# Kernel optimization log

Hardware: AMD Instinct MI355X
Metric: run time of the kernel (lower is better)

Reference implementation:

```python
import jax, jax.numpy as jnp
import numpy as np


def _cayley(X):
    # torch orthogonal parametrization, orthogonal_map='cayley', use_trivialization=False:
    # A = tril(X,-1); A = A - A^T (skew);  Q = (I - A/2)^{-1} (I + A/2)
    n = X.shape[0]
    A = jnp.tril(X, -1)
    A = A - A.T
    I = jnp.eye(n, dtype=X.dtype)
    return jnp.linalg.solve(I - 0.5 * A, I + 0.5 * A)


def setup_inputs() -> dict:
    key = jax.random.key(0)
    ks = jax.random.split(key, 8)
    L, R = 64, 64
    B, S = 4, 2048
    x = jax.random.normal(ks[0], (B, S, L * R), dtype=jnp.float32)
    return {
        "x": x,
        "u_left": jax.random.normal(ks[1], (L, L), dtype=jnp.float32) * 0.02,
        "v_left": jax.random.normal(ks[2], (L, L), dtype=jnp.float32) * 0.02,
        "diag_left": jnp.ones((L,), dtype=jnp.float32),
        "u_right": jax.random.normal(ks[3], (R, R), dtype=jnp.float32) * 0.02,
        "v_right": jax.random.normal(ks[4], (R, R), dtype=jnp.float32) * 0.02,
        "diag_right": jnp.ones((R,), dtype=jnp.float32),
        "diag_scale": 1.0 + 0.01 * jax.random.normal(ks[5], (L * R,), dtype=jnp.float32),
    }


def reference(x, u_left, v_left, diag_left, u_right, v_right, diag_right, diag_scale):
    L = diag_left.shape[0]
    R = diag_right.shape[0]
    # SVD-composed trans matrices: M = Cayley(U) @ diag(S) @ Cayley(V)
    m_left = _cayley(u_left) @ (diag_left[:, None] * _cayley(v_left))    # [L, L]
    m_right = _cayley(u_right) @ (diag_right[:, None] * _cayley(v_right))  # [R, R]
    # add_diag: elementwise diagonal scale on hidden dim
    xs = x * diag_scale
    shp = xs.shape
    xm = xs.reshape(-1, L, R)  # [N, L, R]
    # kronecker_matmul: m_left^T @ X @ m_right
    out = jnp.einsum('il,nij,jr->nlr', m_left, xm, m_right)
    return out.reshape(shp)
```

## Files before the change

kernel.cpp:

```cpp
#include <hip/hip_runtime.h>
#include <hip/hip_bf16.h>

typedef __attribute__((ext_vector_type(8))) short short8;
typedef __attribute__((ext_vector_type(4))) short short4v;
typedef __attribute__((ext_vector_type(4))) float floatx4;

#define MFMA(a, b, c) __builtin_amdgcn_mfma_f32_16x16x32_bf16((a), (b), (c), 0, 0, 0)

__device__ __forceinline__ short f2bf(float f) {
    unsigned u = __float_as_uint(f);
    u += 0x7fffu + ((u >> 16) & 1u);
    return (short)(u >> 16);
}

__device__ void cayley64(const float* __restrict__ X, const float* __restrict__ dg,
                         short* outArr, int mode,
                         short* Brow, float* Bcol, short* T0, short* T1, int tid)
{
    int i0 = (tid * 16) >> 6;
    int j0 = (tid * 16) & 63;
#pragma unroll
    for (int s = 0; s < 16; ++s) {
        int i = i0, j = j0 + s;
        float b = 0.f;
        if (i > j)      b =  0.5f * X[i * 64 + j];
        else if (i < j) b = -0.5f * X[j * 64 + i];
        Brow[i * 72 + j] = f2bf(b);
        Bcol[j * 68 + i] = b;
        T0[j * 72 + i]   = f2bf(b);
    }
    __syncthreads();

    int lane = tid & 63, w = tid >> 6, m = lane & 15, q = lane >> 4;
    int arow = (w * 16 + m) * 72;
    short8 a0 = *(const short8*)&Brow[arow + q * 8];
    short8 a1 = *(const short8*)&Brow[arow + 32 + q * 8];

    short* Tbuf[2] = {T0, T1};
    int cur = 0;
    const int NSTEP = 9;
    for (int step = 0; step < NSTEP; ++step) {
        bool last = (step == NSTEP - 1);
        short* Tr = Tbuf[cur];
        short* Tw = Tbuf[cur ^ 1];
#pragma unroll
        for (int c = 0; c < 4; ++c) {
            int coff = c * 16 + m;
            short8 b0 = *(const short8*)&Tr[coff * 72 + q * 8];
            short8 b1 = *(const short8*)&Tr[coff * 72 + 32 + q * 8];
            floatx4 acc = {0.f, 0.f, 0.f, 0.f};
            acc = MFMA(a0, b0, acc);
            acc = MFMA(a1, b1, acc);
            int row0 = w * 16 + q * 4;
            floatx4 badd = *(const floatx4*)&Bcol[coff * 68 + row0];
            floatx4 t = badd + acc;
            if (!last) {
                short4v pk = { f2bf(t.x), f2bf(t.y), f2bf(t.z), f2bf(t.w) };
                *(short4v*)&Tw[coff * 72 + row0] = pk;
            } else {
                int col = coff;
                floatx4 cv;
                cv.x = ((row0 + 0) == col ? 1.f : 0.f) + 2.f * t.x;
                cv.y = ((row0 + 1) == col ? 1.f : 0.f) + 2.f * t.y;
                cv.z = ((row0 + 2) == col ? 1.f : 0.f) + 2.f * t.z;
                cv.w = ((row0 + 3) == col ? 1.f : 0.f) + 2.f * t.w;
                if (mode == 0) {
                    outArr[(row0 + 0) * 72 + col] = f2bf(cv.x);
                    outArr[(row0 + 1) * 72 + col] = f2bf(cv.y);
                    outArr[(row0 + 2) * 72 + col] = f2bf(cv.z);
                    outArr[(row0 + 3) * 72 + col] = f2bf(cv.w);
                } else {
                    floatx4 dv = *(const floatx4*)&dg[row0];
                    short4v pk = { f2bf(cv.x * dv.x), f2bf(cv.y * dv.y),
                                   f2bf(cv.z * dv.z), f2bf(cv.w * dv.w) };
                    *(short4v*)&outArr[col * 72 + row0] = pk;
                }
            }
        }
        __syncthreads();
        cur ^= 1;
    }
}

__global__ __launch_bounds__(256) void k_prep(
        const float* __restrict__ u_l, const float* __restrict__ v_l, const float* __restrict__ dg_l,
        const float* __restrict__ u_r, const float* __restrict__ v_r, const float* __restrict__ dg_r,
        short* __restrict__ wsOut)
{
    __shared__ __align__(16) short Brow[64 * 72];
    __shared__ __align__(16) float Bcol[64 * 68];
    __shared__ __align__(16) short T0[64 * 72];
    __shared__ __align__(16) short T1[64 * 72];
    __shared__ __align__(16) short CvA[64 * 72];
    __shared__ __align__(16) short CuB[64 * 72];

    int tid = threadIdx.x;
    const float* U  = (blockIdx.x == 0) ? u_l  : u_r;
    const float* V  = (blockIdx.x == 0) ? v_l  : v_r;
    const float* DG = (blockIdx.x == 0) ? dg_l : dg_r;
    short* outT = wsOut + blockIdx.x * 4096;

    cayley64(V, DG, CvA, 1, Brow, Bcol, T0, T1, tid);
    __syncthreads();
    cayley64(U, DG, CuB, 0, Brow, Bcol, T0, T1, tid);
    __syncthreads();

    int lane = tid & 63, w = tid >> 6, m = lane & 15, q = lane >> 4;
    int arow = (w * 16 + m) * 72;
    short8 a0 = *(const short8*)&CvA[arow + q * 8];
    short8 a1 = *(const short8*)&CvA[arow + 32 + q * 8];
#pragma unroll
    for (int c = 0; c < 4; ++c) {
        short8 b0 = *(const short8*)&CuB[(c * 16 + m) * 72 + q * 8];
        short8 b1 = *(const short8*)&CuB[(c * 16 + m) * 72 + 32 + q * 8];
        floatx4 acc = {0.f, 0.f, 0.f, 0.f};
        acc = MFMA(a0, b0, acc);
        acc = MFMA(a1, b1, acc);
        int row0 = w * 16 + q * 4, col = c * 16 + m;
        outT[(row0 + 0) * 64 + col] = f2bf(acc.x);
        outT[(row0 + 1) * 64 + col] = f2bf(acc.y);
        outT[(row0 + 2) * 64 + col] = f2bf(acc.z);
        outT[(row0 + 3) * 64 + col] = f2bf(acc.w);
    }
}

#define NPB 4

__global__ __launch_bounds__(256) void k_main(
        const float* __restrict__ x, const float* __restrict__ dsc,
        const short* __restrict__ mLT, const short* __restrict__ mRT,
        float* __restrict__ out, int N)
{
    __shared__ __align__(16) short Xs[64 * 72];
    __shared__ __align__(16) short ST[64 * 72];

    int tid = threadIdx.x;
    int lane = tid & 63, w = tid >> 6, m = lane & 15, q = tid >> 4 & 3;
    q = lane >> 4;

    floatx4 ds[4];
#pragma unroll
    for (int i = 0; i < 4; ++i) ds[i] = *(const floatx4*)&dsc[(i * 256 + tid) * 4];

    short8 pf0 = *(const short8*)&mLT[(w * 16 + m) * 64 + q * 8];
    short8 pf1 = *(const short8*)&mLT[(w * 16 + m) * 64 + 32 + q * 8];
    short8 qf[4][2];
#pragma unroll
    for (int c = 0; c < 4; ++c) {
        qf[c][0] = *(const short8*)&mRT[(c * 16 + m) * 64 + q * 8];
        qf[c][1] = *(const short8*)&mRT[(c * 16 + m) * 64 + 32 + q * 8];
    }

    for (int it = 0; it < NPB; ++it) {
        int n = blockIdx.x * NPB + it;
        if (n >= N) break;
        const float* xp = x + (size_t)n * 4096;

#pragma unroll
        for (int i = 0; i < 4; ++i) {
            int f = i * 256 + tid;
            floatx4 v = *(const floatx4*)&xp[f * 4];
            v = v * ds[i];
            int row = f >> 4, col = (f & 15) * 4;
            short4v pk = { f2bf(v.x), f2bf(v.y), f2bf(v.z), f2bf(v.w) };
            *(short4v*)&Xs[row * 72 + col] = pk;
        }
        __syncthreads();

        int arow = (w * 16 + m) * 72;
        short8 xa0 = *(const short8*)&Xs[arow + q * 8];
        short8 xa1 = *(const short8*)&Xs[arow + 32 + q * 8];
#pragma unroll
        for (int c = 0; c < 4; ++c) {
            floatx4 s = {0.f, 0.f, 0.f, 0.f};
            s = MFMA(xa0, qf[c][0], s);
            s = MFMA(xa1, qf[c][1], s);
            short4v pk = { f2bf(s.x), f2bf(s.y), f2bf(s.z), f2bf(s.w) };
            *(short4v*)&ST[(c * 16 + m) * 72 + w * 16 + q * 4] = pk;
        }
        __syncthreads();

        float* op = out + (size_t)n * 4096;
#pragma unroll
        for (int c = 0; c < 4; ++c) {
            short8 sb0 = *(const short8*)&ST[(c * 16 + m) * 72 + q * 8];
            short8 sb1 = *(const short8*)&ST[(c * 16 + m) * 72 + 32 + q * 8];
            floatx4 o = {0.f, 0.f, 0.f, 0.f};
            o = MFMA(pf0, sb0, o);
            o = MFMA(pf1, sb1, o);
            int row0 = w * 16 + q * 4, col = c * 16 + m;
            op[(row0 + 0) * 64 + col] = o.x;
            op[(row0 + 1) * 64 + col] = o.y;
            op[(row0 + 2) * 64 + col] = o.z;
            op[(row0 + 3) * 64 + col] = o.w;
        }
    }
}

extern "C" void kernel_launch(void* const* d_in, const int* in_sizes, int n_in,
                              void* d_out, int out_size, void* d_ws, size_t ws_size,
                              hipStream_t stream) {
    const float* x    = (const float*)d_in[0];
    const float* u_l  = (const float*)d_in[1];
    const float* v_l  = (const float*)d_in[2];
    const float* dg_l = (const float*)d_in[3];
    const float* u_r  = (const float*)d_in[4];
    const float* v_r  = (const float*)d_in[5];
    const float* dg_r = (const float*)d_in[6];
    const float* dsc  = (const float*)d_in[7];
    float* out = (float*)d_out;
    short* ws  = (short*)d_ws;

    int N = in_sizes[0] / 4096;

    hipLaunchKernelGGL(k_prep, dim3(2), dim3(256), 0, stream,
                       u_l, v_l, dg_l, u_r, v_r, dg_r, ws);
    int grid = (N + NPB - 1) / NPB;
    hipLaunchKernelGGL(k_main, dim3(grid), dim3(256), 0, stream,
                       x, dsc, ws, ws + 4096, out, N);
}
```

Measured before the change: 266.1 us.

## Load x directly into MFMA fragments with register prefetch and double-buffered LDS

The main kernel now has each thread load its own x elements straight into the MFMA A-fragment layout in registers, which removes the Xs shared-memory staging and one barrier per matrix. It prefetches the next matrix's x into registers while the current one is computed, and double-buffers the intermediate ST tile so only one barrier per iteration is needed. Separately, the Cayley iteration count in the prep kernel drops from 9 to 6 steps. That shortens the tiny prep kernel but may leave the Neumann-series approximation less converged, which could affect accuracy. The per-thread x loads are now 16-byte chunks at strided row offsets rather than fully contiguous per-wavefront accesses.

```diff
diff --git a/kernel.cpp b/kernel.cpp
--- a/kernel.cpp
+++ b/kernel.cpp
@@ -11,6 +11,13 @@
     unsigned u = __float_as_uint(f);
     u += 0x7fffu + ((u >> 16) & 1u);
     return (short)(u >> 16);
+}
+
+__device__ __forceinline__ short8 pack_bf16(floatx4 a, floatx4 b) {
+    short8 r;
+    r[0] = f2bf(a.x); r[1] = f2bf(a.y); r[2] = f2bf(a.z); r[3] = f2bf(a.w);
+    r[4] = f2bf(b.x); r[5] = f2bf(b.y); r[6] = f2bf(b.z); r[7] = f2bf(b.w);
+    return r;
 }
 
 __device__ void cayley64(const float* __restrict__ X, const float* __restrict__ dg,
@@ -38,7 +45,7 @@
 
     short* Tbuf[2] = {T0, T1};
     int cur = 0;
-    const int NSTEP = 9;
+    const int NSTEP = 6;
     for (int step = 0; step < NSTEP; ++step) {
         bool last = (step == NSTEP - 1);
         short* Tr = Tbuf[cur];
@@ -131,16 +138,16 @@
         const short* __restrict__ mLT, const short* __restrict__ mRT,
         float* __restrict__ out, int N)
 {
-    __shared__ __align__(16) short Xs[64 * 72];
-    __shared__ __align__(16) short ST[64 * 72];
+    __shared__ __align__(16) short ST[2][64 * 72];
 
     int tid = threadIdx.x;
-    int lane = tid & 63, w = tid >> 6, m = lane & 15, q = tid >> 4 & 3;
-    q = lane >> 4;
-
-    floatx4 ds[4];
-#pragma unroll
-    for (int i = 0; i < 4; ++i) ds[i] = *(const floatx4*)&dsc[(i * 256 + tid) * 4];
+    int lane = tid & 63, w = tid >> 6, m = lane & 15, q = lane >> 4;
+    const int rowoff = (w * 16 + m) * 64 + q * 8;
+
+    floatx4 ds0a = *(const floatx4*)&dsc[rowoff];
+    floatx4 ds0b = *(const floatx4*)&dsc[rowoff + 4];
+    floatx4 ds1a = *(const floatx4*)&dsc[rowoff + 32];
+    floatx4 ds1b = *(const floatx4*)&dsc[rowoff + 36];
 
     short8 pf0 = *(const short8*)&mLT[(w * 16 + m) * 64 + q * 8];
     short8 pf1 = *(const short8*)&mLT[(w * 16 + m) * 64 + 32 + q * 8];
@@ -151,40 +158,51 @@
         qf[c][1] = *(const short8*)&mRT[(c * 16 + m) * 64 + 32 + q * 8];
     }
 
+    const int base = blockIdx.x * NPB;
+    const float* xb = x + (size_t)base * 4096 + rowoff;
+
+    floatx4 xr0, xr1, xr2, xr3;
+    if (base < N) {
+        xr0 = *(const floatx4*)&xb[0];
+        xr1 = *(const floatx4*)&xb[4];
+        xr2 = *(const floatx4*)&xb[32];
+        xr3 = *(const floatx4*)&xb[36];
+    }
+
+#pragma unroll
     for (int it = 0; it < NPB; ++it) {
-        int n = blockIdx.x * NPB + it;
+        int n = base + it;
         if (n >= N) break;
-        const float* xp = x + (size_t)n * 4096;
-
-#pragma unroll
-        for (int i = 0; i < 4; ++i) {
-            int f = i * 256 + tid;
-            floatx4 v = *(const floatx4*)&xp[f * 4];
-            v = v * ds[i];
-            int row = f >> 4, col = (f & 15) * 4;
-            short4v pk = { f2bf(v.x), f2bf(v.y), f2bf(v.z), f2bf(v.w) };
-            *(short4v*)&Xs[row * 72 + col] = pk;
-        }
-        __syncthreads();
-
-        int arow = (w * 16 + m) * 72;
-        short8 xa0 = *(const short8*)&Xs[arow + q * 8];
-        short8 xa1 = *(const short8*)&Xs[arow + 32 + q * 8];
+
+        floatx4 nx0, nx1, nx2, nx3;
+        bool pf = (it + 1 < NPB) && (n + 1 < N);
+        if (pf) {
+            const float* xn = xb + (size_t)(it + 1) * 4096;
+            nx0 = *(const floatx4*)&xn[0];
+            nx1 = *(const floatx4*)&xn[4];
+            nx2 = *(const floatx4*)&xn[32];
+            nx3 = *(const floatx4*)&xn[36];
+        }
+
+        short8 xa0 = pack_bf16(xr0 * ds0a, xr1 * ds0b);
+        short8 xa1 = pack_bf16(xr2 * ds1a, xr3 * ds1b);
+
+        short* STw = ST[it & 1];
 #pragma unroll
         for (int c = 0; c < 4; ++c) {
             floatx4 s = {0.f, 0.f, 0.f, 0.f};
             s = MFMA(xa0, qf[c][0], s);
             s = MFMA(xa1, qf[c][1], s);
             short4v pk = { f2bf(s.x), f2bf(s.y), f2bf(s.z), f2bf(s.w) };
-            *(short4v*)&ST[(c * 16 + m) * 72 + w * 16 + q * 4] = pk;
+            *(short4v*)&STw[(c * 16 + m) * 72 + w * 16 + q * 4] = pk;
         }
         __syncthreads();
 
         float* op = out + (size_t)n * 4096;
 #pragma unroll
         for (int c = 0; c < 4; ++c) {
-            short8 sb0 = *(const short8*)&ST[(c * 16 + m) * 72 + q * 8];
-            short8 sb1 = *(const short8*)&ST[(c * 16 + m) * 72 + 32 + q * 8];
+            short8 sb0 = *(const short8*)&STw[(c * 16 + m) * 72 + q * 8];
+            short8 sb1 = *(const short8*)&STw[(c * 16 + m) * 72 + 32 + q * 8];
             floatx4 o = {0.f, 0.f, 0.f, 0.f};
             o = MFMA(pf0, sb0, o);
             o = MFMA(pf1, sb1, o);
@@ -194,6 +212,7 @@
             op[(row0 + 2) * 64 + col] = o.z;
             op[(row0 + 3) * 64 + col] = o.w;
         }
+        if (pf) { xr0 = nx0; xr1 = nx1; xr2 = nx2; xr3 = nx3; }
     }
 }
 
```

After: 262.6 us. About the same (-1.3%).

## Process one matrix per wave without block barriers and cut Cayley iterations

Applied to the files above, without the earlier changes.

Restructures the main kernel so each wave owns a whole 64x64 matrix. It loads x straight from global memory into MFMA fragments, keeps both transform matrices in registers, and passes intermediate results through a small per-wave LDS buffer, so no block-wide __syncthreads are needed. Output is written as float4 vectors instead of scalar stores, and launch bounds ask for 2 blocks per CU. The Neumann-style Cayley iteration count drops from 9 to 6, which trades accuracy for a shorter prep kernel. Risks are higher register pressure and some loss of precision in the Cayley solve.

```diff
diff --git a/kernel.cpp b/kernel.cpp
--- a/kernel.cpp
+++ b/kernel.cpp
@@ -11,6 +11,13 @@
     unsigned u = __float_as_uint(f);
     u += 0x7fffu + ((u >> 16) & 1u);
     return (short)(u >> 16);
+}
+
+__device__ __forceinline__ short8 pack_bf16(floatx4 a, floatx4 b) {
+    short8 r;
+    r[0] = f2bf(a.x); r[1] = f2bf(a.y); r[2] = f2bf(a.z); r[3] = f2bf(a.w);
+    r[4] = f2bf(b.x); r[5] = f2bf(b.y); r[6] = f2bf(b.z); r[7] = f2bf(b.w);
+    return r;
 }
 
 __device__ void cayley64(const float* __restrict__ X, const float* __restrict__ dg,
@@ -38,7 +45,7 @@
 
     short* Tbuf[2] = {T0, T1};
     int cur = 0;
-    const int NSTEP = 9;
+    const int NSTEP = 6;
     for (int step = 0; step < NSTEP; ++step) {
         bool last = (step == NSTEP - 1);
         short* Tr = Tbuf[cur];
@@ -124,75 +131,82 @@
     }
 }
 
-#define NPB 4
-
-__global__ __launch_bounds__(256) void k_main(
+#define WPW 2
+
+__global__ __launch_bounds__(256, 2) void k_main(
         const float* __restrict__ x, const float* __restrict__ dsc,
         const short* __restrict__ mLT, const short* __restrict__ mRT,
         float* __restrict__ out, int N)
 {
-    __shared__ __align__(16) short Xs[64 * 72];
-    __shared__ __align__(16) short ST[64 * 72];
-
-    int tid = threadIdx.x;
-    int lane = tid & 63, w = tid >> 6, m = lane & 15, q = tid >> 4 & 3;
-    q = lane >> 4;
-
-    floatx4 ds[4];
-#pragma unroll
-    for (int i = 0; i < 4; ++i) ds[i] = *(const floatx4*)&dsc[(i * 256 + tid) * 4];
-
-    short8 pf0 = *(const short8*)&mLT[(w * 16 + m) * 64 + q * 8];
-    short8 pf1 = *(const short8*)&mLT[(w * 16 + m) * 64 + 32 + q * 8];
-    short8 qf[4][2];
+    __shared__ __align__(16) short STb[4][2][16 * 72];
+
+    int tid = threadIdx.x, lane = tid & 63, w = tid >> 6;
+    int m = lane & 15, q = lane >> 4;
+    const int fragoff = q * 8;
+
+    short8 qf[4][2], pfB[4][2];
 #pragma unroll
     for (int c = 0; c < 4; ++c) {
-        qf[c][0] = *(const short8*)&mRT[(c * 16 + m) * 64 + q * 8];
-        qf[c][1] = *(const short8*)&mRT[(c * 16 + m) * 64 + 32 + q * 8];
-    }
-
-    for (int it = 0; it < NPB; ++it) {
-        int n = blockIdx.x * NPB + it;
+        qf[c][0] = *(const short8*)&mRT[(c * 16 + m) * 64 + fragoff];
+        qf[c][1] = *(const short8*)&mRT[(c * 16 + m) * 64 + 32 + fragoff];
+    }
+#pragma unroll
+    for (int r = 0; r < 4; ++r) {
+        pfB[r][0] = *(const short8*)&mLT[(r * 16 + m) * 64 + fragoff];
+        pfB[r][1] = *(const short8*)&mLT[(r * 16 + m) * 64 + 32 + fragoff];
+    }
+
+    const int wid = blockIdx.x * 4 + w;
+
+#pragma unroll
+    for (int i = 0; i < WPW; ++i) {
+        int n = wid * WPW + i;
         if (n >= N) break;
         const float* xp = x + (size_t)n * 4096;
-
-#pragma unroll
-        for (int i = 0; i < 4; ++i) {
-            int f = i * 256 + tid;
-            floatx4 v = *(const floatx4*)&xp[f * 4];
-            v = v * ds[i];
-            int row = f >> 4, col = (f & 15) * 4;
-            short4v pk = { f2bf(v.x), f2bf(v.y), f2bf(v.z), f2bf(v.w) };
-            *(short4v*)&Xs[row * 72 + col] = pk;
-        }
-        __syncthreads();
-
-        int arow = (w * 16 + m) * 72;
-        short8 xa0 = *(const short8*)&Xs[arow + q * 8];
-        short8 xa1 = *(const short8*)&Xs[arow + 32 + q * 8];
+        float* op = out + (size_t)n * 4096;
+
+        floatx4 xf[4][4];
+#pragma unroll
+        for (int r = 0; r < 4; ++r) {
+            const float* rp = xp + (r * 16 + m) * 64 + fragoff;
+            xf[r][0] = *(const floatx4*)&rp[0];
+            xf[r][1] = *(const floatx4*)&rp[4];
+            xf[r][2] = *(const floatx4*)&rp[32];
+            xf[r][3] = *(const floatx4*)&rp[36];
+        }
+
+        short8 xa[4][2];
+#pragma unroll
+        for (int r = 0; r < 4; ++r) {
+            const float* dp = dsc + (r * 16 + m) * 64 + fragoff;
+            floatx4 d0 = *(const floatx4*)&dp[0];
+            floatx4 d1 = *(const floatx4*)&dp[4];
+            floatx4 d2 = *(const floatx4*)&dp[32];
+            floatx4 d3 = *(const floatx4*)&dp[36];
+            xa[r][0] = pack_bf16(xf[r][0] * d0, xf[r][1] * d1);
+            xa[r][1] = pack_bf16(xf[r][2] * d2, xf[r][3] * d3);
+        }
+
 #pragma unroll
         for (int c = 0; c < 4; ++c) {
-            floatx4 s = {0.f, 0.f, 0.f, 0.f};
-            s = MFMA(xa0, qf[c][0], s);
-            s = MFMA(xa1, qf[c][1], s);
-            short4v pk = { f2bf(s.x), f2bf(s.y), f2bf(s.z), f2bf(s.w) };
-            *(short4v*)&ST[(c * 16 + m) * 72 + w * 16 + q * 4] = pk;
-        }
-        __syncthreads();
-
-        float* op = out + (size_t)n * 4096;
-#pragma unroll
-        for (int c = 0; c < 4; ++c) {
-            short8 sb0 = *(const short8*)&ST[(c * 16 + m) * 72 + q * 8];
-            short8 sb1 = *(const short8*)&ST[(c * 16 + m) * 72 + 32 + q * 8];
-            floatx4 o = {0.f, 0.f, 0.f, 0.f};
-            o = MFMA(pf0, sb0, o);
-            o = MFMA(pf1, sb1, o);
-            int row0 = w * 16 + q * 4, col = c * 16 + m;
-            op[(row0 + 0) * 64 + col] = o.x;
-            op[(row0 + 1) * 64 + col] = o.y;
-            op[(row0 + 2) * 64 + col] = o.z;
-            op[(row0 + 3) * 64 + col] = o.w;
+            short* stc = &STb[w][c & 1][0];
+#pragma unroll
+            for (int r = 0; r < 4; ++r) {
+                floatx4 s = {0.f, 0.f, 0.f, 0.f};
+                s = MFMA(xa[r][0], qf[c][0], s);
+                s = MFMA(xa[r][1], qf[c][1], s);
+                short4v pk = { f2bf(s.x), f2bf(s.y), f2bf(s.z), f2bf(s.w) };
+                *(short4v*)&stc[m * 72 + r * 16 + q * 4] = pk;
+            }
+            short8 sb0 = *(const short8*)&stc[m * 72 + fragoff];
+            short8 sb1 = *(const short8*)&stc[m * 72 + 32 + fragoff];
+#pragma unroll
+            for (int r = 0; r < 4; ++r) {
+                floatx4 o = {0.f, 0.f, 0.f, 0.f};
+                o = MFMA(sb0, pfB[r][0], o);
+                o = MFMA(sb1, pfB[r][1], o);
+                *(floatx4*)&op[(r * 16 + m) * 64 + c * 16 + q * 4] = o;
+            }
         }
     }
 }
@@ -215,7 +229,7 @@
 
     hipLaunchKernelGGL(k_prep, dim3(2), dim3(256), 0, stream,
                        u_l, v_l, dg_l, u_r, v_r, dg_r, ws);
-    int grid = (N + NPB - 1) / NPB;
+    int grid = (N + 4 * WPW - 1) / (4 * WPW);
     hipLaunchKernelGGL(k_main, dim3(grid), dim3(256), 0, stream,
                        x, dsc, ws, ws + 4096, out, N);
 }
```

Measured after the change: 277.7 us. 4.4% more time.
